# Performance work log

Measured on AMD Instinct MI355X. Metric: run time of the kernel, lower is better.

## Reference

```python
import jax, jax.numpy as jnp
import numpy as np

BN_EPS = 1e-5

def setup_inputs() -> dict:
    key = jax.random.key(0)
    k0, k1, k2, k3, k4 = jax.random.split(key, 5)
    B, N, D, E = 8, 256, 128, 4096
    x_l = jax.random.normal(k0, (B, N, D), dtype=jnp.float32)
    src = jax.random.randint(k1, (E,), 0, N)
    dst = jax.random.randint(k2, (E,), 0, N)
    edge_index_l = jnp.stack([src, dst], axis=0)  # [2, E]
    mask_l = jax.random.randint(k3, (B, N), 0, 2).astype(bool)
    W = jax.random.normal(k4, (D, D), dtype=jnp.float32) * (1.0 / np.sqrt(D))
    b = jnp.zeros((D,), jnp.float32)
    gamma = jnp.ones((D,), jnp.float32)
    beta = jnp.zeros((D,), jnp.float32)
    return {"x_l": x_l, "edge_index_l": edge_index_l, "mask_l": mask_l,
            "W": W, "b": b, "gamma": gamma, "beta": beta}


def reference(x_l, edge_index_l, mask_l, W, b, gamma, beta):
    # x_l: [B, N, D]; edge_index_l: [2, E]; mask_l: [B, N] bool
    B, N, D = x_l.shape
    src, dst = edge_index_l[0], edge_index_l[1]
    # Vectorized replacement of the Python edge loop: edges with dst - src == 3
    # zero the mask at both endpoints (the explicit interaction zeroing in the
    # original is subsumed by the mask, since masked entries never survive).
    cov = (dst - src) == 3  # [E] bool
    hit = jnp.zeros((N,), bool)
    hit = hit.at[src].max(cov)
    hit = hit.at[dst].max(cov)
    mask = mask_l & ~hit[None, :]  # [B, N]
    # Pairwise mask: outer AND minus diagonal
    eye = jnp.eye(N, dtype=bool)
    pair_mask = (mask[:, :, None] & mask[:, None, :]) & ~eye[None]  # [B, N, N]
    # Outer-product interaction: [B, N, N, D]
    interaction = x_l[:, :, None, :] * x_l[:, None, :, :]
    # Linear
    h = jnp.einsum('bijd,ed->bije', interaction, W) + b
    # BatchNorm1d over the masked (selected) rows, training-mode batch stats.
    m = pair_mask[..., None].astype(h.dtype)  # [B, N, N, 1]
    cnt = jnp.maximum(jnp.sum(m), 1.0)
    mean = jnp.sum(h * m, axis=(0, 1, 2)) / cnt  # [D]
    var = jnp.sum(m * (h - mean) ** 2, axis=(0, 1, 2)) / cnt  # biased, as torch BN
    hn = (h - mean) * jax.lax.rsqrt(var + BN_EPS) * gamma + beta
    # Dropout is identity in eval mode; LeakyReLU slope 0.01 (torch default).
    out = jax.nn.leaky_relu(hn, negative_slope=0.01) * m  # zero non-selected entries
    return out, pair_mask
```

## Files before the change

kernel.cpp:

```cpp
#include <hip/hip_runtime.h>

#define B_ 8
#define N_ 256
#define D_ 128
#define E_ 4096

typedef __attribute__((ext_vector_type(8))) short bf16x8;
typedef __attribute__((ext_vector_type(4))) float f32x4;

__device__ inline unsigned int pack2bf(float lo, float hi) {
    unsigned ul = __float_as_uint(lo);
    ul = ul + 0x7FFFu + ((ul >> 16) & 1u);
    unsigned uh = __float_as_uint(hi);
    uh = uh + 0x7FFFu + ((uh >> 16) & 1u);
    return (ul >> 16) | (uh & 0xFFFF0000u);
}

__device__ inline unsigned short f2bf(float f) {
    unsigned u = __float_as_uint(f);
    u = u + 0x7FFFu + ((u >> 16) & 1u);
    return (unsigned short)(u >> 16);
}


__global__ __launch_bounds__(256) void k_prep(const void* __restrict__ edges_raw,
                                              const void* __restrict__ mask_raw,
                                              const float* __restrict__ W,
                                              int* __restrict__ mask,
                                              int* __restrict__ jlist,
                                              int* __restrict__ jcnt,
                                              unsigned short* __restrict__ Wb,
                                              float* __restrict__ Wt,
                                              float* __restrict__ tq,
                                              float* __restrict__ dq) {
    int blk = blockIdx.x, tid = threadIdx.x;
    if (blk >= B_) {
        int idx = (blk - B_) * 256 + tid;
        if (idx < 16384) {
            float w = W[idx];
            Wb[idx] = f2bf(w);
            int e = idx >> 7, d = idx & 127;
            Wt[d * D_ + e] = w;
        } else if (idx < 16512) tq[idx - 16384] = 0.0f;
        else dq[idx - 16512] = 0.0f;
        return;
    }
    int b = blk;
    __shared__ unsigned char hit[N_];
    __shared__ int flags[2];
    __shared__ int wcnt[4], wbase[4];
    hit[tid] = 0;
    if (tid < 2) flags[tid] = 0;
    __syncthreads();

    const unsigned char* mb = (const unsigned char*)mask_raw;
    int loc_m = 0;
    for (int idx = tid; idx < B_ * N_; idx += 256)
        if ((idx & 3) && mb[idx]) loc_m = 1;
    if (loc_m) flags[0] = 1;
    const int* e32 = (const int*)edges_raw;
    int loc_e = 0;
    for (int idx = tid; idx < 2 * E_; idx += 256)
        if ((idx & 1) && e32[idx]) loc_e = 1;
    if (loc_e) flags[1] = 1;
    __syncthreads();

    int mask_is_u8 = flags[0], e_is_i32 = flags[1];
    const long long* e64 = (const long long*)edges_raw;
    for (int e = tid; e < E_; e += 256) {
        int s, d;
        if (e_is_i32) { s = e32[e]; d = e32[E_ + e]; }
        else          { s = (int)e64[e]; d = (int)e64[E_ + e]; }
        if (d - s == 3) { hit[s] = 1; hit[d] = 1; }
    }
    __syncthreads();

    const int* m32 = (const int*)mask_raw;
    int lane = tid & 63, wid = tid >> 6;
    int raw = mask_is_u8 ? (int)(mb[b * N_ + tid] != 0) : (int)(m32[b * N_ + tid] != 0);
    int m = raw && (hit[tid] == 0);
    mask[b * N_ + tid] = m;
    unsigned long long bal = __ballot(m);
    if (lane == 0) wcnt[wid] = __popcll(bal);
    __syncthreads();
    if (tid == 0) {
        int base = 0;
        for (int w = 0; w < 4; ++w) { wbase[w] = base; base += wcnt[w]; }
        jcnt[b] = base;
    }
    __syncthreads();
    if (m) {
        int pos = wbase[wid] + __popcll(bal & ((1ull << lane) - 1ull));
        jlist[b * N_ + pos] = tid;
    }
}

__global__ __launch_bounds__(128) void k_gram3(const float* __restrict__ x,
                                               const int* __restrict__ jlist,
                                               const int* __restrict__ jcnt,
                                               float* __restrict__ part,
                                               float* __restrict__ s1,
                                               float* __restrict__ cdiag) {
    int d = blockIdx.x, b = blockIdx.y, dp = threadIdx.x;
    int kc = jcnt[b];
    const int* jl = jlist + b * N_;
    const float* xb = x + (size_t)b * N_ * D_;
    float c0 = 0, c1 = 0, q0 = 0, q1 = 0, s0 = 0, s1a = 0;
    int t = 0;
    for (; t + 1 < kc; t += 2) {
        int i0 = jl[t], i1 = jl[t + 1];
        float xd0 = xb[i0 * D_ + d], xp0 = xb[i0 * D_ + dp];
        float xd1 = xb[i1 * D_ + d], xp1 = xb[i1 * D_ + dp];
        c0 += xd0 * xp0; q0 += (xd0 * xd0) * (xp0 * xp0); s0 += xd0;
        c1 += xd1 * xp1; q1 += (xd1 * xd1) * (xp1 * xp1); s1a += xd1;
    }
    if (t < kc) {
        int i0 = jl[t];
        float xd0 = xb[i0 * D_ + d], xp0 = xb[i0 * D_ + dp];
        c0 += xd0 * xp0; q0 += (xd0 * xd0) * (xp0 * xp0); s0 += xd0;
    }
    float c = c0 + c1, q = q0 + q1, sa = s0 + s1a;
    part[((size_t)b * D_ + d) * D_ + dp] = c * c - q;
    if (dp == d) cdiag[b * D_ + d] = c;
    if (dp == 0) s1[b * D_ + d] = sa;
}

__global__ __launch_bounds__(128) void k_mw2(const float* __restrict__ part,
                                             const float* __restrict__ Wt,
                                             const float* __restrict__ s1,
                                             const float* __restrict__ cdiag,
                                             float* __restrict__ tq,
                                             float* __restrict__ dq) {
    __shared__ float Ms[D_];
    __shared__ float svs;
    int d = blockIdx.x, e = threadIdx.x;
    float m = 0.0f;
#pragma unroll
    for (int b = 0; b < B_; ++b) m += part[((size_t)b * D_ + d) * D_ + e];
    Ms[e] = m;
    if (e == 0) {
        float sv = 0.0f;
#pragma unroll
        for (int b = 0; b < B_; ++b) {
            float s = s1[b * D_ + d];
            sv += s * s - cdiag[b * D_ + d];
        }
        svs = sv;
    }
    __syncthreads();
    float y = 0.0f;
#pragma unroll 8
    for (int p = 0; p < D_; ++p) y += Ms[p] * Wt[p * D_ + e];
    float wed = Wt[d * D_ + e];
    atomicAdd(tq + e, wed * y);
    atomicAdd(dq + e, wed * svs);
}

__global__ __launch_bounds__(256) void k_main(const float* __restrict__ x,
                                              const int* __restrict__ mask,
                                              const int* __restrict__ jlist,
                                              const int* __restrict__ jcnt,
                                              const unsigned short* __restrict__ Wb,
                                              const float* __restrict__ tq,
                                              const float* __restrict__ dq,
                                              const float* __restrict__ bvec,
                                              const float* __restrict__ gamma,
                                              const float* __restrict__ beta,
                                              float* __restrict__ out,
                                              float* __restrict__ pair) {
    __shared__ int msk[N_];
    __shared__ __align__(16) unsigned char Vsb[64 * 256];
    __shared__ float scs[D_], shs[D_];

    int b = blockIdx.y, i = blockIdx.x;
    int tid = threadIdx.x;
    msk[tid] = mask[b * N_ + tid];
    __syncthreads();
    int mi = msk[i];

    float pm = (mi && msk[tid] && tid != i) ? 1.0f : 0.0f;
    pair[(size_t)(b * N_ + i) * N_ + tid] = pm;

    float4 z4 = make_float4(0.f, 0.f, 0.f, 0.f);
    float4* outrow = (float4*)(out + (size_t)(b * N_ + i) * N_ * D_);

    if (!mi) {
        for (int k = tid; k < N_ * D_ / 4; k += 256) outrow[k] = z4;
        return;
    }

    {
        int c = tid & 31, g = tid >> 5;
        for (int j = g; j < N_; j += 8)
            if (!msk[j] || j == i) outrow[j * 32 + c] = z4;
    }

    if (tid < D_) {
        float cnt = 0.0f;
#pragma unroll
        for (int bb = 0; bb < B_; ++bb) {
            float k = (float)jcnt[bb];
            cnt += k * k - k;
        }
        if (cnt < 1.0f) cnt = 1.0f;
        float be = bvec[tid];
        float mean = dq[tid] / cnt + be;
        float eh2 = tq[tid] / cnt + 2.0f * be * mean - be * be;
        float var = eh2 - mean * mean;
        if (var < 0.0f) var = 0.0f;
        float s = gamma[tid] * rsqrtf(var + 1e-5f);
        scs[tid] = s;
        shs[tid] = be * s + beta[tid] - mean * s;
    }

    int w = tid >> 6, l = tid & 63;
    int lo16 = l & 15, hi4 = l >> 4;
    int E0 = w * 32;

    bf16x8 bfrag[2][4];
#pragma unroll
    for (int et = 0; et < 2; ++et) {
        int e = E0 + 2 * lo16 + et;
#pragma unroll
        for (int ks = 0; ks < 4; ++ks)
            bfrag[et][ks] = *(const bf16x8*)(Wb + (size_t)e * D_ + ks * 32 + hi4 * 8);
    }

    int kc = jcnt[b];
    const int* jl = jlist + b * N_;
    const float* xi = x + (size_t)(b * N_ + i) * D_;
    float* outbase = out + (size_t)(b * N_ + i) * N_ * D_;

    for (int jt = 0; jt < kc; jt += 64) {
        __syncthreads();
        int jn = kc - jt; if (jn > 64) jn = 64;

        {
            int r = tid >> 2, q = tid & 3;
            int jrow = jt + r;
            bool ok = (r < jn);
            const float* xj = ok ? (x + (size_t)(b * N_ + jl[jrow]) * D_) : xi;
            int d0 = q * 32;
#pragma unroll
            for (int c4 = 0; c4 < 4; ++c4) {
                int d = d0 + c4 * 8;
                float4 a0 = *(const float4*)(xj + d);
                float4 a1 = *(const float4*)(xj + d + 4);
                float4 b0 = *(const float4*)(xi + d);
                float4 b1 = *(const float4*)(xi + d + 4);
                uint4 pk;
                pk.x = pack2bf(a0.x * b0.x, a0.y * b0.y);
                pk.y = pack2bf(a0.z * b0.z, a0.w * b0.w);
                pk.z = pack2bf(a1.x * b1.x, a1.y * b1.y);
                pk.w = pack2bf(a1.z * b1.z, a1.w * b1.w);
                if (!ok) pk = make_uint4(0u, 0u, 0u, 0u);
                int byte = r * 256 + ((d * 2) ^ ((r & 7) << 4));
                *(uint4*)(Vsb + byte) = pk;
            }
        }
        __syncthreads();

        f32x4 acc[4][2];
#pragma unroll
        for (int jq = 0; jq < 4; ++jq) {
            acc[jq][0] = (f32x4)(0.f);
            acc[jq][1] = (f32x4)(0.f);
            int rA = jq * 16 + lo16;
            int rbase = rA * 256;
            int rx = (rA & 7) << 4;
            bf16x8 a0 = *(const bf16x8*)(Vsb + rbase + (((hi4 * 8) * 2) ^ rx));
            bf16x8 a1 = *(const bf16x8*)(Vsb + rbase + (((32 + hi4 * 8) * 2) ^ rx));
            bf16x8 a2 = *(const bf16x8*)(Vsb + rbase + (((64 + hi4 * 8) * 2) ^ rx));
            bf16x8 a3 = *(const bf16x8*)(Vsb + rbase + (((96 + hi4 * 8) * 2) ^ rx));
            acc[jq][0] = __builtin_amdgcn_mfma_f32_16x16x32_bf16(a0, bfrag[0][0], acc[jq][0], 0, 0, 0);
            acc[jq][1] = __builtin_amdgcn_mfma_f32_16x16x32_bf16(a0, bfrag[1][0], acc[jq][1], 0, 0, 0);
            acc[jq][0] = __builtin_amdgcn_mfma_f32_16x16x32_bf16(a1, bfrag[0][1], acc[jq][0], 0, 0, 0);
            acc[jq][1] = __builtin_amdgcn_mfma_f32_16x16x32_bf16(a1, bfrag[1][1], acc[jq][1], 0, 0, 0);
            acc[jq][0] = __builtin_amdgcn_mfma_f32_16x16x32_bf16(a2, bfrag[0][2], acc[jq][0], 0, 0, 0);
            acc[jq][1] = __builtin_amdgcn_mfma_f32_16x16x32_bf16(a2, bfrag[1][2], acc[jq][1], 0, 0, 0);
            acc[jq][0] = __builtin_amdgcn_mfma_f32_16x16x32_bf16(a3, bfrag[0][3], acc[jq][0], 0, 0, 0);
            acc[jq][1] = __builtin_amdgcn_mfma_f32_16x16x32_bf16(a3, bfrag[1][3], acc[jq][1], 0, 0, 0);
        }

        float sc0 = scs[E0 + 2 * lo16], sh0 = shs[E0 + 2 * lo16];
        float sc1 = scs[E0 + 2 * lo16 + 1], sh1 = shs[E0 + 2 * lo16 + 1];
#pragma unroll
        for (int jq = 0; jq < 4; ++jq) {
#pragma unroll
            for (int v = 0; v < 4; ++v) {
                int jrow = jt + jq * 16 + hi4 * 4 + v;
                if (jrow < kc) {
                    int j = jl[jrow];
                    if (j != i) {
                        float h0 = acc[jq][0][v] * sc0 + sh0;
                        float h1 = acc[jq][1][v] * sc1 + sh1;
                        float2 o;
                        o.x = h0 >= 0.f ? h0 : 0.01f * h0;
                        o.y = h1 >= 0.f ? h1 : 0.01f * h1;
                        *(float2*)(outbase + (size_t)j * D_ + E0 + 2 * lo16) = o;
                    }
                }
            }
        }
    }
}

extern "C" void kernel_launch(void* const* d_in, const int* in_sizes, int n_in,
                              void* d_out, int out_size, void* d_ws, size_t ws_size,
                              hipStream_t stream) {
    const float* x = (const float*)d_in[0];
    const void* edges = d_in[1];
    const void* mask_in = d_in[2];
    const float* W = (const float*)d_in[3];
    const float* bvec = (const float*)d_in[4];
    const float* gamma = (const float*)d_in[5];
    const float* beta = (const float*)d_in[6];

    float* out = (float*)d_out;
    float* pair = out + (size_t)B_ * N_ * N_ * D_;

    char* ws = (char*)d_ws;
    int* mask = (int*)(ws + 0);
    int* jlist = (int*)(ws + 8192);
    int* jcnt = (int*)(ws + 16384);
    float* tq = (float*)(ws + 16448);
    float* dq = (float*)(ws + 16960);
    unsigned short* Wb = (unsigned short*)(ws + 17472);
    float* Wt = (float*)(ws + 50240);
    float* s1 = (float*)(ws + 115776);
    float* cdiag = (float*)(ws + 119872);
    float* part = (float*)(ws + 123968);

    k_prep<<<73, 256, 0, stream>>>(edges, mask_in, W, mask, jlist, jcnt, Wb, Wt, tq, dq);
    {
        dim3 g(D_, B_);
        k_gram3<<<g, 128, 0, stream>>>(x, jlist, jcnt, part, s1, cdiag);
    }
    k_mw2<<<128, 128, 0, stream>>>(part, Wt, s1, cdiag, tq, dq);
    {
        dim3 g(N_, B_);
        k_main<<<g, 256, 0, stream>>>(x, mask, jlist, jcnt, Wb, tq, dq, bvec, gamma, beta, out, pair);
    }
}
```

Before: 108.9 us.

## Split output zero-fill into separate blocks of a merged mega-kernel grid

Output zeroing for masked pairs moves out of the per-row compute blocks into 8192 dedicated lightweight blocks, each covering 64 (i,j) rows. These are prepended to the compute blocks in a single 1D launch. The aim is better load balance: fully masked rows no longer leave one block writing 128KB of zeros while other blocks do GEMM work, so zero stores spread across the GPU and overlap with compute. The cost is extra block-scheduling overhead and repeated mask reads.

```diff
diff --git a/kernel.cpp b/kernel.cpp
--- a/kernel.cpp
+++ b/kernel.cpp
@@ -156,7 +156,8 @@
     atomicAdd(dq + e, wed * svs);
 }
 
-__global__ __launch_bounds__(256) void k_main(const float* __restrict__ x,
+#define NZBLK 8192
+__global__ __launch_bounds__(256) void k_mega(const float* __restrict__ x,
                                               const int* __restrict__ mask,
                                               const int* __restrict__ jlist,
                                               const int* __restrict__ jcnt,
@@ -168,12 +169,38 @@
                                               const float* __restrict__ beta,
                                               float* __restrict__ out,
                                               float* __restrict__ pair) {
+    int blk = blockIdx.x, tid = threadIdx.x;
+
+    if (blk < NZBLK) {
+        __shared__ int zf[64];
+        int r0 = blk * 64;
+        int j0 = r0 & 255;
+        int i = (r0 >> 8) & 255;
+        int b = r0 >> 16;
+        int mi = mask[b * N_ + i];
+        if (tid < 64) {
+            int j = j0 + tid;
+            int mj = mask[b * N_ + j];
+            zf[tid] = (!mi || !mj || j == i) ? 1 : 0;
+        }
+        __syncthreads();
+        float4 z4 = make_float4(0.f, 0.f, 0.f, 0.f);
+        float4* base = (float4*)(out + ((size_t)(b * N_ + i) * N_ + j0) * D_);
+        int c = tid & 31, g = tid >> 5;
+#pragma unroll
+        for (int p = 0; p < 8; ++p) {
+            int s = g + 8 * p;
+            if (zf[s]) base[s * 32 + c] = z4;
+        }
+        return;
+    }
+
     __shared__ int msk[N_];
     __shared__ __align__(16) unsigned char Vsb[64 * 256];
     __shared__ float scs[D_], shs[D_];
 
-    int b = blockIdx.y, i = blockIdx.x;
-    int tid = threadIdx.x;
+    int cblk = blk - NZBLK;
+    int b = cblk >> 8, i = cblk & 255;
     msk[tid] = mask[b * N_ + tid];
     __syncthreads();
     int mi = msk[i];
@@ -181,19 +208,7 @@
     float pm = (mi && msk[tid] && tid != i) ? 1.0f : 0.0f;
     pair[(size_t)(b * N_ + i) * N_ + tid] = pm;
 
-    float4 z4 = make_float4(0.f, 0.f, 0.f, 0.f);
-    float4* outrow = (float4*)(out + (size_t)(b * N_ + i) * N_ * D_);
-
-    if (!mi) {
-        for (int k = tid; k < N_ * D_ / 4; k += 256) outrow[k] = z4;
-        return;
-    }
-
-    {
-        int c = tid & 31, g = tid >> 5;
-        for (int j = g; j < N_; j += 8)
-            if (!msk[j] || j == i) outrow[j * 32 + c] = z4;
-    }
+    if (!mi) return;
 
     if (tid < D_) {
         float cnt = 0.0f;
@@ -337,8 +352,6 @@
         k_gram3<<<g, 128, 0, stream>>>(x, jlist, jcnt, part, s1, cdiag);
     }
     k_mw2<<<128, 128, 0, stream>>>(part, Wt, s1, cdiag, tq, dq);
-    {
-        dim3 g(N_, B_);
-        k_main<<<g, 256, 0, stream>>>(x, mask, jlist, jcnt, Wb, tq, dq, bvec, gamma, beta, out, pair);
-    }
-}
+    k_mega<<<NZBLK + B_ * N_, 256, 0, stream>>>(x, mask, jlist, jcnt, Wb, tq, dq,
+                                                bvec, gamma, beta, out, pair);
+}
```

Result: slower. 120.6 us (+10.8%).
